# Performance work log

Hardware: AMD Instinct MI355X
Metric: run time of the kernel (lower is better)

The kernel has to match this reference:

```python
import jax, jax.numpy as jnp
import numpy as np

N = 170000      # nodes (ogbn-arxiv scale)
E = 2720000     # edges (avg degree 16)
IN, H, L, OUT = 128, 256, 4, 40
BN_EPS = 1e-5


def setup_inputs() -> dict:
    key = jax.random.key(0)
    ks = jax.random.split(key, 6)
    x = jax.random.normal(ks[0], (N, IN), jnp.float32)
    edge_index = jax.random.randint(ks[1], (2, E), 0, N, dtype=jnp.int64)
    W_in = jax.random.normal(ks[2], (IN, H), jnp.float32) * 0.05
    b_in = jnp.zeros((H,), jnp.float32)
    W_hid = jax.random.normal(ks[3], (L - 1, H, H), jnp.float32) * 0.05
    b_hid = jnp.zeros((L - 1, H), jnp.float32)
    gamma = jnp.ones((L, H), jnp.float32)
    beta = jnp.zeros((L, H), jnp.float32)
    W_out = jax.random.normal(ks[4], (L * H, OUT), jnp.float32) * 0.05
    b_out = jnp.zeros((OUT,), jnp.float32)
    return dict(x=x, edge_index=edge_index, W_in=W_in, b_in=b_in,
                W_hid=W_hid, b_hid=b_hid, gamma=gamma, beta=beta,
                W_out=W_out, b_out=b_out)


def _gcn_aggregate(h, src, dst, norm_e, inv_deg):
    # message passing with symmetric normalization + self-loop term
    msg = h[src] * norm_e[:, None]                      # [E, H] gather
    agg = jax.ops.segment_sum(msg, dst, num_segments=N)  # [N, H] scatter-add
    return agg + h * inv_deg[:, None]                   # self-loop: deg^-1


def reference(x, edge_index, W_in, b_in, W_hid, b_hid, gamma, beta, W_out, b_out):
    src, dst = edge_index[0], edge_index[1]
    # degree (incl. self-loop), PyG gcn_norm style
    deg = jax.ops.segment_sum(jnp.ones((E,), x.dtype), dst, num_segments=N) + 1.0
    dinv = jax.lax.rsqrt(deg)
    norm_e = dinv[src] * dinv[dst]
    inv_deg = 1.0 / deg

    outs = []
    h = x
    for i in range(L):
        W = W_in if i == 0 else W_hid[i - 1]
        b = b_in if i == 0 else b_hid[i - 1]
        h = _gcn_aggregate(h @ W, src, dst, norm_e, inv_deg) + b
        # BatchNorm1d (training-mode batch statistics, biased variance)
        mean = jnp.mean(h, axis=0)
        var = jnp.mean(jnp.square(h - mean), axis=0)
        h = (h - mean) * jax.lax.rsqrt(var + BN_EPS) * gamma[i] + beta[i]
        h = jax.nn.relu(h)  # dropout is identity in eval mode
        outs.append(h)

    z = jnp.concatenate(outs, axis=-1) @ W_out + b_out  # JK 'cat' -> [N, L*H] @ [L*H, OUT]
    return jax.nn.log_softmax(z, axis=-1)
```

## Files before the change

### kernel.cpp

```cpp
#include <hip/hip_runtime.h>
#include <math.h>

constexpr int kN = 170000;
constexpr int kE = 2720000;
constexpr int kFin = 128;
constexpr int kFh = 256;
constexpr int kL = 4;
constexpr int kFout = 40;

typedef __attribute__((ext_vector_type(8))) short bf16x8;
typedef __attribute__((ext_vector_type(4))) float f32x4;

__device__ __forceinline__ float jk_b2f(unsigned short u) {
    unsigned int x = ((unsigned int)u) << 16;
    float f;
    __builtin_memcpy(&f, &x, 4);
    return f;
}
__device__ __forceinline__ unsigned short jk_f2b(float f) {
    unsigned int x;
    __builtin_memcpy(&x, &f, 4);
    unsigned int r = (x + 0x7fffu + ((x >> 16) & 1u)) >> 16;
    return (unsigned short)r;
}

union U4 {
    uint4 v;
    unsigned short s[8];
};

__global__ void jk7_zero_i(int* p, int n) {
    int i = blockIdx.x * blockDim.x + threadIdx.x;
    if (i < n) p[i] = 0;
}
__global__ void jk7_zero_f(float* p, int n) {
    int i = blockIdx.x * blockDim.x + threadIdx.x;
    if (i < n) p[i] = 0.0f;
}

__global__ void jk7_detect(const int* eb, int* flag) {
    __shared__ int nz;
    if (threadIdx.x == 0) nz = 0;
    __syncthreads();
    int bad = 0;
    for (int j = 0; j < 4; j++) {
        int idx = threadIdx.x * 4 + j;
        if (eb[2 * idx + 1] != 0) bad = 1;
    }
    if (bad) atomicOr(&nz, 1);
    __syncthreads();
    if (threadIdx.x == 0) {
        flag[0] = nz ? 0 : 1;
        flag[1] = 0;
    }
}

__global__ void jk7_count(const int* eb, const int* flag, int* counts, int* rank) {
    int e = blockIdx.x * blockDim.x + threadIdx.x;
    if (e >= kE) return;
    int s64 = flag[0];
    int d = eb[(kE + e) << s64];
    rank[e] = atomicAdd(&counts[d], 1);
}

__global__ void jk7_nodeprep(const int* counts, float* dinv, float* invdeg, int* off,
                             int* cursor) {
    int n = blockIdx.x * blockDim.x + threadIdx.x;
    if (n < kN) {
        int c = counts[n];
        float deg = (float)c + 1.0f;
        dinv[n] = rsqrtf(deg);
        invdeg[n] = 1.0f / deg;
        off[n] = atomicAdd(cursor, c);
    }
}

__global__ void jk7_fill(const int* eb, const int* flag, const int* rank, const int* off,
                         const float* dinv, int2* csr) {
    int e = blockIdx.x * blockDim.x + threadIdx.x;
    if (e >= kE) return;
    int s64 = flag[0];
    int s = eb[e << s64];
    int d = eb[(kE + e) << s64];
    int p = off[d] + rank[e];
    float w = dinv[s] * dinv[d];
    csr[p] = make_int2(s, __float_as_int(w));
}

__global__ void jk7_wt(const float* W, unsigned short* Wt, int K) {
    int idx = blockIdx.x * blockDim.x + threadIdx.x;
    if (idx >= K * kFh) return;
    int c = idx / K, k = idx % K;
    Wt[idx] = jk_f2b(W[(size_t)k * kFh + c]);
}

__global__ void jk7_wtout(const float* Wout, unsigned short* Wto) {
    int idx = blockIdx.x * blockDim.x + threadIdx.x;
    if (idx >= kL * 48 * 256) return;
    int l = idx / (48 * 256);
    int rem = idx % (48 * 256);
    int col = rem >> 8, k = rem & 255;
    float wv = (col < kFout) ? Wout[(size_t)(l * kFh + k) * kFout + col] : 0.f;
    unsigned short hi = jk_f2b(wv);
    float res = wv - jk_b2f(hi);
    unsigned short lo = jk_f2b(res);
    Wto[((size_t)(l * 2 + 0) * 48 + col) * 256 + k] = hi;
    Wto[((size_t)(l * 2 + 1) * 48 + col) * 256 + k] = lo;
}

template <int MODE>
__global__ __launch_bounds__(256) void jk7_gemm(const void* Aptr, const unsigned short* Wt,
                                                unsigned short* C, int K, const float* sc,
                                                const float* sh) {
    __shared__ unsigned short As[128][40];
    __shared__ unsigned short Bs[128][40];
    __shared__ float ssc[256], ssh[256];
    int tid = threadIdx.x;
    if (MODE == 1) {
        ssc[tid] = sc[tid];
        ssh[tid] = sh[tid];
    }
    __syncthreads();
    int row0 = blockIdx.x * 128;
    int n0 = blockIdx.y * 128;
    int lane = tid & 63, w = tid >> 6;
    int wm = w >> 1, wn = w & 1;
    int lr = lane & 15, lg = lane >> 4;

    f32x4 acc[4][4];
#pragma unroll
    for (int i = 0; i < 4; i++)
#pragma unroll
        for (int j = 0; j < 4; j++) acc[i][j] = (f32x4){0.f, 0.f, 0.f, 0.f};

    int sr = tid >> 1;
    int skh = (tid & 1) * 16;

    for (int k0 = 0; k0 < K; k0 += 32) {
        {
            int row = row0 + sr;
            if (MODE == 0) {
                const float* A = (const float*)Aptr;
                unsigned short tmp[16];
                if (row < kN) {
                    const float* g = A + (size_t)row * K + k0 + skh;
#pragma unroll
                    for (int j = 0; j < 16; j++) tmp[j] = jk_f2b(g[j]);
                } else {
#pragma unroll
                    for (int j = 0; j < 16; j++) tmp[j] = 0;
                }
                *(uint4*)&As[sr][skh] = *(uint4*)&tmp[0];
                *(uint4*)&As[sr][skh + 8] = *(uint4*)&tmp[8];
            } else {
                const unsigned short* A = (const unsigned short*)Aptr;
                U4 o0, o1;
                if (row < kN) {
                    U4 u0, u1;
                    const unsigned short* g = A + (size_t)row * K + k0 + skh;
                    u0.v = *(const uint4*)g;
                    u1.v = *(const uint4*)(g + 8);
#pragma unroll
                    for (int j = 0; j < 8; j++) {
                        float v = jk_b2f(u0.s[j]) * ssc[k0 + skh + j] + ssh[k0 + skh + j];
                        o0.s[j] = jk_f2b(v > 0.f ? v : 0.f);
                    }
#pragma unroll
                    for (int j = 0; j < 8; j++) {
                        float v = jk_b2f(u1.s[j]) * ssc[k0 + skh + 8 + j] + ssh[k0 + skh + 8 + j];
                        o1.s[j] = jk_f2b(v > 0.f ? v : 0.f);
                    }
                } else {
#pragma unroll
                    for (int j = 0; j < 8; j++) { o0.s[j] = 0; o1.s[j] = 0; }
                }
                *(uint4*)&As[sr][skh] = o0.v;
                *(uint4*)&As[sr][skh + 8] = o1.v;
            }
        }
        {
            const unsigned short* g = Wt + (size_t)(n0 + sr) * K + k0 + skh;
            *(uint4*)&Bs[sr][skh] = *(const uint4*)g;
            *(uint4*)&Bs[sr][skh + 8] = *(const uint4*)(g + 8);
        }
        __syncthreads();

        bf16x8 af[4], bfr[4];
#pragma unroll
        for (int mi = 0; mi < 4; mi++)
            af[mi] = *(const bf16x8*)&As[wm * 64 + mi * 16 + lr][lg * 8];
#pragma unroll
        for (int ni = 0; ni < 4; ni++)
            bfr[ni] = *(const bf16x8*)&Bs[wn * 64 + ni * 16 + lr][lg * 8];
#pragma unroll
        for (int mi = 0; mi < 4; mi++)
#pragma unroll
            for (int ni = 0; ni < 4; ni++)
                acc[mi][ni] = __builtin_amdgcn_mfma_f32_16x16x32_bf16(af[mi], bfr[ni],
                                                                      acc[mi][ni], 0, 0, 0);
        __syncthreads();
    }

#pragma unroll
    for (int mi = 0; mi < 4; mi++) {
#pragma unroll
        for (int j = 0; j < 4; j++) {
            int row = row0 + wm * 64 + mi * 16 + lg * 4 + j;
            if (row < kN) {
#pragma unroll
                for (int ni = 0; ni < 4; ni++) {
                    int col = n0 + wn * 64 + ni * 16 + lr;
                    C[(size_t)row * kFh + col] = jk_f2b(acc[mi][ni][j]);
                }
            }
        }
    }
}

__global__ __launch_bounds__(256) void jk7_agg(const unsigned short* t, const float* bias,
                                               const int* off, const int* cnt, const int2* csr,
                                               const float* invdeg, unsigned short* h) {
    int n = blockIdx.x * 8 + (threadIdx.x >> 5);
    if (n >= kN) return;
    int c0 = (threadIdx.x & 31) * 8;

    float acc[8];
    {
        U4 u;
        u.v = *(const uint4*)(t + (size_t)n * kFh + c0);
        float sw = invdeg[n];
#pragma unroll
        for (int j = 0; j < 8; j++) acc[j] = sw * jk_b2f(u.s[j]);
    }

    int base = off[n], c = cnt[n];
    for (int i = 0; i < c; i += 4) {
        float w[4];
        U4 uu[4];
#pragma unroll
        for (int q = 0; q < 4; q++) {
            int e = i + q;
            bool v = e < c;
            int2 cw = csr[v ? base + e : base];
            w[q] = v ? __int_as_float(cw.y) : 0.0f;
            uu[q].v = *(const uint4*)(t + (size_t)cw.x * kFh + c0);
        }
#pragma unroll
        for (int q = 0; q < 4; q++)
#pragma unroll
            for (int j = 0; j < 8; j++) acc[j] += w[q] * jk_b2f(uu[q].s[j]);
    }

    U4 o;
#pragma unroll
    for (int j = 0; j < 8; j++) o.s[j] = jk_f2b(acc[j] + bias[c0 + j]);
    *(uint4*)(h + (size_t)n * kFh + c0) = o.v;
}

__global__ __launch_bounds__(256) void jk7_bnstats(const unsigned short* h, float* stats) {
    __shared__ float lsum[256], lsq[256];
    int tid = threadIdx.x;
    lsum[tid] = 0.f;
    lsq[tid] = 0.f;
    __syncthreads();
    int c0 = (tid & 31) * 8;
    int grp = tid >> 5;
    float rs[8] = {}, rq[8] = {};
    for (int n = blockIdx.x * 8 + grp; n < kN; n += gridDim.x * 8) {
        U4 u;
        u.v = *(const uint4*)(h + (size_t)n * kFh + c0);
#pragma unroll
        for (int j = 0; j < 8; j++) {
            float v = jk_b2f(u.s[j]);
            rs[j] += v;
            rq[j] += v * v;
        }
    }
#pragma unroll
    for (int j = 0; j < 8; j++) {
        atomicAdd(&lsum[c0 + j], rs[j]);
        atomicAdd(&lsq[c0 + j], rq[j]);
    }
    __syncthreads();
    atomicAdd(&stats[tid], lsum[tid]);
    atomicAdd(&stats[256 + tid], lsq[tid]);
}

__global__ void jk7_bnfinal(const float* stats, const float* gamma, const float* beta, int layer,
                            float* scale, float* shift) {
    int c = threadIdx.x;
    float mean = stats[c] / (float)kN;
    float var = stats[256 + c] / (float)kN - mean * mean;
    var = var < 0.f ? 0.f : var;
    float sc = gamma[layer * kFh + c] * rsqrtf(var + 1e-5f);
    scale[c] = sc;
    shift[c] = beta[layer * kFh + c] - mean * sc;
}

template <int FIRST, int LAST>
__global__ __launch_bounds__(256) void jk7_zacc(const unsigned short* h, const float* scale,
                                                const float* shift, const unsigned short* Wto,
                                                const float* bout, float* z, float* out) {
    __shared__ unsigned short Bs[2][48][264];
    __shared__ unsigned short As[128][40];
    __shared__ float ssc[256], ssh[256];
    int tid = threadIdx.x;
    for (int f = tid; f < 2 * 48 * 256; f += 256) {
        int hl = f / (48 * 256);
        int rem = f % (48 * 256);
        Bs[hl][rem >> 8][rem & 255] = Wto[f];
    }
    ssc[tid] = scale[tid];
    ssh[tid] = shift[tid];
    __syncthreads();

    int row0 = blockIdx.x * 128;
    int w = tid >> 6, lane = tid & 63;
    int lr = lane & 15, lg = lane >> 4;
    int sr = tid >> 1, skh = (tid & 1) * 16;

    f32x4 acc[2][3];
#pragma unroll
    for (int mi = 0; mi < 2; mi++)
#pragma unroll
        for (int ni = 0; ni < 3; ni++) acc[mi][ni] = (f32x4){0.f, 0.f, 0.f, 0.f};

    for (int k0 = 0; k0 < kFh; k0 += 32) {
        int row = row0 + sr;
        U4 o0, o1;
        if (row < kN) {
            U4 u0, u1;
            const unsigned short* g = h + (size_t)row * kFh + k0 + skh;
            u0.v = *(const uint4*)g;
            u1.v = *(const uint4*)(g + 8);
#pragma unroll
            for (int j = 0; j < 8; j++) {
                float v = jk_b2f(u0.s[j]) * ssc[k0 + skh + j] + ssh[k0 + skh + j];
                o0.s[j] = jk_f2b(v > 0.f ? v : 0.f);
            }
#pragma unroll
            for (int j = 0; j < 8; j++) {
                float v = jk_b2f(u1.s[j]) * ssc[k0 + skh + 8 + j] + ssh[k0 + skh + 8 + j];
                o1.s[j] = jk_f2b(v > 0.f ? v : 0.f);
            }
        } else {
#pragma unroll
            for (int j = 0; j < 8; j++) { o0.s[j] = 0; o1.s[j] = 0; }
        }
        *(uint4*)&As[sr][skh] = o0.v;
        *(uint4*)&As[sr][skh + 8] = o1.v;
        __syncthreads();

        bf16x8 af[2], bh[3], bl[3];
#pragma unroll
        for (int mi = 0; mi < 2; mi++)
            af[mi] = *(const bf16x8*)&As[w * 32 + mi * 16 + lr][lg * 8];
#pragma unroll
        for (int ni = 0; ni < 3; ni++) {
            bh[ni] = *(const bf16x8*)&Bs[0][ni * 16 + lr][k0 + lg * 8];
            bl[ni] = *(const bf16x8*)&Bs[1][ni * 16 + lr][k0 + lg * 8];
        }
#pragma unroll
        for (int mi = 0; mi < 2; mi++)
#pragma unroll
            for (int ni = 0; ni < 3; ni++) {
                acc[mi][ni] = __builtin_amdgcn_mfma_f32_16x16x32_bf16(af[mi], bh[ni],
                                                                      acc[mi][ni], 0, 0, 0);
                acc[mi][ni] = __builtin_amdgcn_mfma_f32_16x16x32_bf16(af[mi], bl[ni],
                                                                      acc[mi][ni], 0, 0, 0);
            }
        __syncthreads();
    }

#pragma unroll
    for (int mi = 0; mi < 2; mi++) {
#pragma unroll
        for (int j = 0; j < 4; j++) {
            int row = row0 + w * 32 + mi * 16 + lg * 4 + j;
            if (row >= kN) continue;
            if (!LAST) {
#pragma unroll
                for (int ni = 0; ni < 3; ni++) {
                    int col = ni * 16 + lr;
                    if (col < kFout) {
                        if (FIRST)
                            z[(size_t)row * kFout + col] = acc[mi][ni][j] + bout[col];
                        else
                            z[(size_t)row * kFout + col] += acc[mi][ni][j];
                    }
                }
            } else {
                const float* zp = z + (size_t)row * kFout;
                float v0 = zp[lr] + acc[mi][0][j];
                float v1 = zp[16 + lr] + acc[mi][1][j];
                float v2 = (lr < 8) ? (zp[32 + lr] + acc[mi][2][j]) : -1e30f;
                float m = fmaxf(fmaxf(v0, v1), v2);
                m = fmaxf(m, __shfl_xor(m, 1, 64));
                m = fmaxf(m, __shfl_xor(m, 2, 64));
                m = fmaxf(m, __shfl_xor(m, 4, 64));
                m = fmaxf(m, __shfl_xor(m, 8, 64));
                float s = expf(v0 - m) + expf(v1 - m) + ((lr < 8) ? expf(v2 - m) : 0.f);
                s += __shfl_xor(s, 1, 64);
                s += __shfl_xor(s, 2, 64);
                s += __shfl_xor(s, 4, 64);
                s += __shfl_xor(s, 8, 64);
                float ls = m + logf(s);
                float* op = out + (size_t)row * kFout;
                op[lr] = v0 - ls;
                op[16 + lr] = v1 - ls;
                if (lr < 8) op[32 + lr] = v2 - ls;
            }
        }
    }
}

extern "C" void kernel_launch(void* const* d_in, const int* in_sizes, int n_in,
                              void* d_out, int out_size, void* d_ws, size_t ws_size,
                              hipStream_t stream) {
    (void)in_sizes; (void)n_in; (void)out_size; (void)ws_size;
    const float* x = (const float*)d_in[0];
    const int* eb = (const int*)d_in[1];
    const float* W_in = (const float*)d_in[2];
    const float* b_in = (const float*)d_in[3];
    const float* W_hid = (const float*)d_in[4];
    const float* b_hid = (const float*)d_in[5];
    const float* gamma = (const float*)d_in[6];
    const float* beta = (const float*)d_in[7];
    const float* W_out = (const float*)d_in[8];
    const float* b_out = (const float*)d_in[9];
    float* out = (float*)d_out;

    char* p = (char*)d_ws;
    auto alloc = [&](size_t b) -> void* {
        void* r = (void*)p;
        p += (b + 255) & ~(size_t)255;
        return r;
    };
    int* flag = (int*)alloc(8);
    int* counts = (int*)alloc((size_t)kN * 4);
    int* off = (int*)alloc((size_t)kN * 4);
    float* dinv = (float*)alloc((size_t)kN * 4);
    float* invdeg = (float*)alloc((size_t)kN * 4);
    float* bnsums = (float*)alloc((size_t)kL * 512 * 4);
    float* bnss = (float*)alloc((size_t)kL * 512 * 4);
    int* rank = (int*)alloc((size_t)kE * 4);
    int2* csr = (int2*)alloc((size_t)kE * 8);
    unsigned short* hA = (unsigned short*)alloc((size_t)kN * kFh * 2);
    unsigned short* hB = (unsigned short*)alloc((size_t)kN * kFh * 2);
    float* z = (float*)alloc((size_t)kN * kFout * 4);
    unsigned short* Wt0 = (unsigned short*)alloc((size_t)kFin * kFh * 2);
    unsigned short* Wt1 = (unsigned short*)alloc((size_t)kFh * kFh * 2);
    unsigned short* Wt2 = (unsigned short*)alloc((size_t)kFh * kFh * 2);
    unsigned short* Wt3 = (unsigned short*)alloc((size_t)kFh * kFh * 2);
    unsigned short* Wto = (unsigned short*)alloc((size_t)kL * 2 * 48 * 256 * 2);

    jk7_zero_i<<<(kN + 255) / 256, 256, 0, stream>>>(counts, kN);
    jk7_zero_f<<<(kL * 512 + 255) / 256, 256, 0, stream>>>(bnsums, kL * 512);
    jk7_detect<<<1, 256, 0, stream>>>(eb, flag);
    jk7_count<<<(kE + 255) / 256, 256, 0, stream>>>(eb, flag, counts, rank);
    jk7_nodeprep<<<(kN + 255) / 256, 256, 0, stream>>>(counts, dinv, invdeg, off, flag + 1);
    jk7_fill<<<(kE + 255) / 256, 256, 0, stream>>>(eb, flag, rank, off, dinv, csr);

    jk7_wt<<<(kFin * kFh + 255) / 256, 256, 0, stream>>>(W_in, Wt0, kFin);
    jk7_wt<<<(kFh * kFh + 255) / 256, 256, 0, stream>>>(W_hid, Wt1, kFh);
    jk7_wt<<<(kFh * kFh + 255) / 256, 256, 0, stream>>>(W_hid + (size_t)kFh * kFh, Wt2, kFh);
    jk7_wt<<<(kFh * kFh + 255) / 256, 256, 0, stream>>>(W_hid + (size_t)2 * kFh * kFh, Wt3, kFh);
    jk7_wtout<<<(kL * 48 * 256 + 255) / 256, 256, 0, stream>>>(W_out, Wto);

    unsigned short* Wts[4] = {Wt0, Wt1, Wt2, Wt3};
    dim3 gg((kN + 127) / 128, 2);
    int zg = (kN + 127) / 128;
    for (int l = 0; l < kL; l++) {
        const float* b = (l == 0) ? b_in : b_hid + (size_t)(l - 1) * kFh;
        int K = (l == 0) ? kFin : kFh;
        if (l == 0) {
            jk7_gemm<0><<<gg, 256, 0, stream>>>(x, Wts[l], hA, K, nullptr, nullptr);
        } else {
            float* scp = bnss + (size_t)(l - 1) * 512;
            jk7_gemm<1><<<gg, 256, 0, stream>>>(hB, Wts[l], hA, K, scp, scp + 256);
        }
        jk7_agg<<<(kN + 7) / 8, 256, 0, stream>>>(hA, b, off, counts, csr, invdeg, hB);
        jk7_bnstats<<<1024, 256, 0, stream>>>(hB, bnsums + (size_t)l * 512);
        jk7_bnfinal<<<1, 256, 0, stream>>>(bnsums + (size_t)l * 512, gamma, beta, l,
                                           bnss + (size_t)l * 512, bnss + (size_t)l * 512 + 256);
        const unsigned short* wtl = Wto + (size_t)l * 2 * 48 * 256;
        float* sc = bnss + (size_t)l * 512;
        if (l == 0)
            jk7_zacc<1, 0><<<zg, 256, 0, stream>>>(hB, sc, sc + 256, wtl, b_out, z, out);
        else if (l < kL - 1)
            jk7_zacc<0, 0><<<zg, 256, 0, stream>>>(hB, sc, sc + 256, wtl, b_out, z, out);
        else
            jk7_zacc<0, 1><<<zg, 256, 0, stream>>>(hB, sc, sc + 256, wtl, b_out, z, out);
    }
}
```

Baseline: 1.759 ms.

## Aggregate before GEMM in first layer, vectorize CSR build, merge weight prep

Layer 0 now aggregates over the 128-wide bf16 input before multiplying by W_in, using linearity, so the gather runs over 128 channels instead of 256. The input bias is folded into the GEMM epilogue. The count and fill kernels handle four edges per thread with vector loads. The weight transposes are merged into one launch, and x is converted to bf16 once up front. Together these cut gather traffic and launch count, at the price of a changed rounding order (bf16 aggregation before the GEMM).

```diff
diff --git a/kernel.cpp b/kernel.cpp
--- a/kernel.cpp
+++ b/kernel.cpp
@@ -28,17 +28,21 @@
     uint4 v;
     unsigned short s[8];
 };
-
-__global__ void jk7_zero_i(int* p, int n) {
+union U2 {
+    uint2 v;
+    unsigned short s[4];
+};
+
+__global__ void jk8_zero_i(int* p, int n) {
     int i = blockIdx.x * blockDim.x + threadIdx.x;
     if (i < n) p[i] = 0;
 }
-__global__ void jk7_zero_f(float* p, int n) {
+__global__ void jk8_zero_f(float* p, int n) {
     int i = blockIdx.x * blockDim.x + threadIdx.x;
     if (i < n) p[i] = 0.0f;
 }
 
-__global__ void jk7_detect(const int* eb, int* flag) {
+__global__ void jk8_detect(const int* eb, int* flag) {
     __shared__ int nz;
     if (threadIdx.x == 0) nz = 0;
     __syncthreads();
@@ -55,15 +59,26 @@
     }
 }
 
-__global__ void jk7_count(const int* eb, const int* flag, int* counts, int* rank) {
-    int e = blockIdx.x * blockDim.x + threadIdx.x;
-    if (e >= kE) return;
+__global__ void jk8_count(const int* eb, const int* flag, int* counts, int* rank) {
+    int e0 = (blockIdx.x * blockDim.x + threadIdx.x) * 4;
+    if (e0 >= kE) return;
     int s64 = flag[0];
-    int d = eb[(kE + e) << s64];
-    rank[e] = atomicAdd(&counts[d], 1);
-}
-
-__global__ void jk7_nodeprep(const int* counts, float* dinv, float* invdeg, int* off,
+    int d[4];
+    if (s64) {
+        int4 c1 = *(const int4*)(eb + 2 * ((size_t)kE + e0));
+        int4 c2 = *(const int4*)(eb + 2 * ((size_t)kE + e0) + 4);
+        d[0] = c1.x; d[1] = c1.z; d[2] = c2.x; d[3] = c2.z;
+    } else {
+        int4 c1 = *(const int4*)(eb + (size_t)kE + e0);
+        d[0] = c1.x; d[1] = c1.y; d[2] = c1.z; d[3] = c1.w;
+    }
+    int r[4];
+#pragma unroll
+    for (int q = 0; q < 4; q++) r[q] = atomicAdd(&counts[d[q]], 1);
+    *(int4*)(rank + e0) = make_int4(r[0], r[1], r[2], r[3]);
+}
+
+__global__ void jk8_nodeprep(const int* counts, float* dinv, float* invdeg, int* off,
                              int* cursor) {
     int n = blockIdx.x * blockDim.x + threadIdx.x;
     if (n < kN) {
@@ -75,43 +90,73 @@
     }
 }
 
-__global__ void jk7_fill(const int* eb, const int* flag, const int* rank, const int* off,
+__global__ void jk8_fill(const int* eb, const int* flag, const int* rank, const int* off,
                          const float* dinv, int2* csr) {
-    int e = blockIdx.x * blockDim.x + threadIdx.x;
-    if (e >= kE) return;
+    int e0 = (blockIdx.x * blockDim.x + threadIdx.x) * 4;
+    if (e0 >= kE) return;
     int s64 = flag[0];
-    int s = eb[e << s64];
-    int d = eb[(kE + e) << s64];
-    int p = off[d] + rank[e];
-    float w = dinv[s] * dinv[d];
-    csr[p] = make_int2(s, __float_as_int(w));
-}
-
-__global__ void jk7_wt(const float* W, unsigned short* Wt, int K) {
+    int s[4], d[4];
+    if (s64) {
+        int4 a1 = *(const int4*)(eb + 2 * (size_t)e0);
+        int4 a2 = *(const int4*)(eb + 2 * (size_t)e0 + 4);
+        s[0] = a1.x; s[1] = a1.z; s[2] = a2.x; s[3] = a2.z;
+        int4 c1 = *(const int4*)(eb + 2 * ((size_t)kE + e0));
+        int4 c2 = *(const int4*)(eb + 2 * ((size_t)kE + e0) + 4);
+        d[0] = c1.x; d[1] = c1.z; d[2] = c2.x; d[3] = c2.z;
+    } else {
+        int4 a1 = *(const int4*)(eb + (size_t)e0);
+        s[0] = a1.x; s[1] = a1.y; s[2] = a1.z; s[3] = a1.w;
+        int4 c1 = *(const int4*)(eb + (size_t)kE + e0);
+        d[0] = c1.x; d[1] = c1.y; d[2] = c1.z; d[3] = c1.w;
+    }
+    int4 rr = *(const int4*)(rank + e0);
+    int r[4] = {rr.x, rr.y, rr.z, rr.w};
+#pragma unroll
+    for (int q = 0; q < 4; q++) {
+        int p = off[d[q]] + r[q];
+        float w = dinv[s[q]] * dinv[d[q]];
+        csr[p] = make_int2(s[q], __float_as_int(w));
+    }
+}
+
+__global__ void jk8_prepw(const float* W_in, const float* W_hid, const float* Wout,
+                          unsigned short* Wt0, unsigned short* Wt1, unsigned short* Wto) {
     int idx = blockIdx.x * blockDim.x + threadIdx.x;
-    if (idx >= K * kFh) return;
-    int c = idx / K, k = idx % K;
-    Wt[idx] = jk_f2b(W[(size_t)k * kFh + c]);
-}
-
-__global__ void jk7_wtout(const float* Wout, unsigned short* Wto) {
-    int idx = blockIdx.x * blockDim.x + threadIdx.x;
-    if (idx >= kL * 48 * 256) return;
-    int l = idx / (48 * 256);
-    int rem = idx % (48 * 256);
-    int col = rem >> 8, k = rem & 255;
-    float wv = (col < kFout) ? Wout[(size_t)(l * kFh + k) * kFout + col] : 0.f;
-    unsigned short hi = jk_f2b(wv);
-    float res = wv - jk_b2f(hi);
-    unsigned short lo = jk_f2b(res);
-    Wto[((size_t)(l * 2 + 0) * 48 + col) * 256 + k] = hi;
-    Wto[((size_t)(l * 2 + 1) * 48 + col) * 256 + k] = lo;
+    if (idx < 32768) {
+        int c = idx >> 7, k = idx & 127;
+        Wt0[idx] = jk_f2b(W_in[(size_t)k * kFh + c]);
+    } else if (idx < 32768 + 196608) {
+        int t2 = idx - 32768;
+        int l = t2 >> 16, rem = t2 & 65535;
+        int c = rem >> 8, k = rem & 255;
+        Wt1[(size_t)l * 65536 + rem] = jk_f2b(W_hid[(size_t)l * 65536 + k * kFh + c]);
+    } else if (idx < 32768 + 196608 + 49152) {
+        int t2 = idx - 32768 - 196608;
+        int l = t2 / (48 * 256), rem = t2 % (48 * 256);
+        int col = rem >> 8, k = rem & 255;
+        float wv = (col < kFout) ? Wout[(size_t)(l * kFh + k) * kFout + col] : 0.f;
+        unsigned short hi = jk_f2b(wv);
+        unsigned short lo = jk_f2b(wv - jk_b2f(hi));
+        Wto[((size_t)(l * 2 + 0) * 48 + col) * 256 + k] = hi;
+        Wto[((size_t)(l * 2 + 1) * 48 + col) * 256 + k] = lo;
+    }
+}
+
+__global__ void jk8_xb(const float* x, unsigned short* xb) {
+    int i = blockIdx.x * blockDim.x + threadIdx.x;
+    if (i >= kN * kFin / 8) return;
+    float4 a = *(const float4*)(x + (size_t)i * 8);
+    float4 b = *(const float4*)(x + (size_t)i * 8 + 4);
+    U4 o;
+    o.s[0] = jk_f2b(a.x); o.s[1] = jk_f2b(a.y); o.s[2] = jk_f2b(a.z); o.s[3] = jk_f2b(a.w);
+    o.s[4] = jk_f2b(b.x); o.s[5] = jk_f2b(b.y); o.s[6] = jk_f2b(b.z); o.s[7] = jk_f2b(b.w);
+    *(uint4*)(xb + (size_t)i * 8) = o.v;
 }
 
 template <int MODE>
-__global__ __launch_bounds__(256) void jk7_gemm(const void* Aptr, const unsigned short* Wt,
+__global__ __launch_bounds__(256) void jk8_gemm(const unsigned short* A, const unsigned short* Wt,
                                                 unsigned short* C, int K, const float* sc,
-                                                const float* sh) {
+                                                const float* sh, const float* bias) {
     __shared__ unsigned short As[128][40];
     __shared__ unsigned short Bs[128][40];
     __shared__ float ssc[256], ssh[256];
@@ -119,6 +164,8 @@
     if (MODE == 1) {
         ssc[tid] = sc[tid];
         ssh[tid] = sh[tid];
+    } else {
+        ssc[tid] = bias[tid];
     }
     __syncthreads();
     int row0 = blockIdx.x * 128;
@@ -140,20 +187,15 @@
         {
             int row = row0 + sr;
             if (MODE == 0) {
-                const float* A = (const float*)Aptr;
-                unsigned short tmp[16];
+                uint4 u0 = make_uint4(0, 0, 0, 0), u1 = make_uint4(0, 0, 0, 0);
                 if (row < kN) {
-                    const float* g = A + (size_t)row * K + k0 + skh;
-#pragma unroll
-                    for (int j = 0; j < 16; j++) tmp[j] = jk_f2b(g[j]);
-                } else {
-#pragma unroll
-                    for (int j = 0; j < 16; j++) tmp[j] = 0;
+                    const unsigned short* g = A + (size_t)row * K + k0 + skh;
+                    u0 = *(const uint4*)g;
+                    u1 = *(const uint4*)(g + 8);
                 }
-                *(uint4*)&As[sr][skh] = *(uint4*)&tmp[0];
-                *(uint4*)&As[sr][skh + 8] = *(uint4*)&tmp[8];
+                *(uint4*)&As[sr][skh] = u0;
+                *(uint4*)&As[sr][skh + 8] = u1;
             } else {
-                const unsigned short* A = (const unsigned short*)Aptr;
                 U4 o0, o1;
                 if (row < kN) {
                     U4 u0, u1;
@@ -210,54 +252,85 @@
 #pragma unroll
                 for (int ni = 0; ni < 4; ni++) {
                     int col = n0 + wn * 64 + ni * 16 + lr;
-                    C[(size_t)row * kFh + col] = jk_f2b(acc[mi][ni][j]);
+                    float v = acc[mi][ni][j];
+                    if (MODE == 0) v += ssc[col];
+                    C[(size_t)row * kFh + col] = jk_f2b(v);
                 }
             }
         }
     }
 }
 
-__global__ __launch_bounds__(256) void jk7_agg(const unsigned short* t, const float* bias,
+template <int CH, int HASB>
+__global__ __launch_bounds__(256) void jk8_agg(const unsigned short* t, const float* bias,
                                                const int* off, const int* cnt, const int2* csr,
                                                const float* invdeg, unsigned short* h) {
+    constexpr int PC = CH / 32;
+    constexpr int DEPTH = (CH == 128) ? 8 : 6;
     int n = blockIdx.x * 8 + (threadIdx.x >> 5);
     if (n >= kN) return;
-    int c0 = (threadIdx.x & 31) * 8;
-
-    float acc[8];
+    int c0 = (threadIdx.x & 31) * PC;
+
+    float acc[PC];
     {
-        U4 u;
-        u.v = *(const uint4*)(t + (size_t)n * kFh + c0);
         float sw = invdeg[n];
-#pragma unroll
-        for (int j = 0; j < 8; j++) acc[j] = sw * jk_b2f(u.s[j]);
+        if constexpr (PC == 8) {
+            U4 u;
+            u.v = *(const uint4*)(t + (size_t)n * CH + c0);
+#pragma unroll
+            for (int j = 0; j < 8; j++) acc[j] = sw * jk_b2f(u.s[j]);
+        } else {
+            U2 u;
+            u.v = *(const uint2*)(t + (size_t)n * CH + c0);
+#pragma unroll
+            for (int j = 0; j < 4; j++) acc[j] = sw * jk_b2f(u.s[j]);
+        }
     }
 
     int base = off[n], c = cnt[n];
-    for (int i = 0; i < c; i += 4) {
-        float w[4];
-        U4 uu[4];
-#pragma unroll
-        for (int q = 0; q < 4; q++) {
+    for (int i = 0; i < c; i += DEPTH) {
+        float w[DEPTH];
+        U4 u8[PC == 8 ? DEPTH : 1];
+        U2 u4[PC == 4 ? DEPTH : 1];
+#pragma unroll
+        for (int q = 0; q < DEPTH; q++) {
             int e = i + q;
             bool v = e < c;
             int2 cw = csr[v ? base + e : base];
             w[q] = v ? __int_as_float(cw.y) : 0.0f;
-            uu[q].v = *(const uint4*)(t + (size_t)cw.x * kFh + c0);
-        }
-#pragma unroll
-        for (int q = 0; q < 4; q++)
-#pragma unroll
-            for (int j = 0; j < 8; j++) acc[j] += w[q] * jk_b2f(uu[q].s[j]);
-    }
-
-    U4 o;
-#pragma unroll
-    for (int j = 0; j < 8; j++) o.s[j] = jk_f2b(acc[j] + bias[c0 + j]);
-    *(uint4*)(h + (size_t)n * kFh + c0) = o.v;
-}
-
-__global__ __launch_bounds__(256) void jk7_bnstats(const unsigned short* h, float* stats) {
+            if constexpr (PC == 8)
+                u8[q].v = *(const uint4*)(t + (size_t)cw.x * CH + c0);
+            else
+                u4[q].v = *(const uint2*)(t + (size_t)cw.x * CH + c0);
+        }
+#pragma unroll
+        for (int q = 0; q < DEPTH; q++) {
+            if constexpr (PC == 8) {
+#pragma unroll
+                for (int j = 0; j < 8; j++) acc[j] += w[q] * jk_b2f(u8[q].s[j]);
+            } else {
+#pragma unroll
+                for (int j = 0; j < 4; j++) acc[j] += w[q] * jk_b2f(u4[q].s[j]);
+            }
+        }
+    }
+
+    if constexpr (PC == 8) {
+        U4 o;
+#pragma unroll
+        for (int j = 0; j < 8; j++)
+            o.s[j] = jk_f2b(HASB ? acc[j] + bias[c0 + j] : acc[j]);
+        *(uint4*)(h + (size_t)n * CH + c0) = o.v;
+    } else {
+        U2 o;
+#pragma unroll
+        for (int j = 0; j < 4; j++)
+            o.s[j] = jk_f2b(HASB ? acc[j] + bias[c0 + j] : acc[j]);
+        *(uint2*)(h + (size_t)n * CH + c0) = o.v;
+    }
+}
+
+__global__ __launch_bounds__(256) void jk8_bnstats(const unsigned short* h, float* stats) {
     __shared__ float lsum[256], lsq[256];
     int tid = threadIdx.x;
     lsum[tid] = 0.f;
@@ -286,7 +359,7 @@
     atomicAdd(&stats[256 + tid], lsq[tid]);
 }
 
-__global__ void jk7_bnfinal(const float* stats, const float* gamma, const float* beta, int layer,
+__global__ void jk8_bnfinal(const float* stats, const float* gamma, const float* beta, int layer,
                             float* scale, float* shift) {
     int c = threadIdx.x;
     float mean = stats[c] / (float)kN;
@@ -298,7 +371,7 @@
 }
 
 template <int FIRST, int LAST>
-__global__ __launch_bounds__(256) void jk7_zacc(const unsigned short* h, const float* scale,
+__global__ __launch_bounds__(256) void jk8_zacc(const unsigned short* h, const float* scale,
                                                 const float* shift, const unsigned short* Wto,
                                                 const float* bout, float* z, float* out) {
     __shared__ unsigned short Bs[2][48][264];
@@ -449,47 +522,43 @@
     unsigned short* hB = (unsigned short*)alloc((size_t)kN * kFh * 2);
     float* z = (float*)alloc((size_t)kN * kFout * 4);
     unsigned short* Wt0 = (unsigned short*)alloc((size_t)kFin * kFh * 2);
-    unsigned short* Wt1 = (unsigned short*)alloc((size_t)kFh * kFh * 2);
-    unsigned short* Wt2 = (unsigned short*)alloc((size_t)kFh * kFh * 2);
-    unsigned short* Wt3 = (unsigned short*)alloc((size_t)kFh * kFh * 2);
+    unsigned short* Wt1 = (unsigned short*)alloc((size_t)3 * kFh * kFh * 2);
     unsigned short* Wto = (unsigned short*)alloc((size_t)kL * 2 * 48 * 256 * 2);
 
-    jk7_zero_i<<<(kN + 255) / 256, 256, 0, stream>>>(counts, kN);
-    jk7_zero_f<<<(kL * 512 + 255) / 256, 256, 0, stream>>>(bnsums, kL * 512);
-    jk7_detect<<<1, 256, 0, stream>>>(eb, flag);
-    jk7_count<<<(kE + 255) / 256, 256, 0, stream>>>(eb, flag, counts, rank);
-    jk7_nodeprep<<<(kN + 255) / 256, 256, 0, stream>>>(counts, dinv, invdeg, off, flag + 1);
-    jk7_fill<<<(kE + 255) / 256, 256, 0, stream>>>(eb, flag, rank, off, dinv, csr);
-
-    jk7_wt<<<(kFin * kFh + 255) / 256, 256, 0, stream>>>(W_in, Wt0, kFin);
-    jk7_wt<<<(kFh * kFh + 255) / 256, 256, 0, stream>>>(W_hid, Wt1, kFh);
-    jk7_wt<<<(kFh * kFh + 255) / 256, 256, 0, stream>>>(W_hid + (size_t)kFh * kFh, Wt2, kFh);
-    jk7_wt<<<(kFh * kFh + 255) / 256, 256, 0, stream>>>(W_hid + (size_t)2 * kFh * kFh, Wt3, kFh);
-    jk7_wtout<<<(kL * 48 * 256 + 255) / 256, 256, 0, stream>>>(W_out, Wto);
-
-    unsigned short* Wts[4] = {Wt0, Wt1, Wt2, Wt3};
+    jk8_zero_i<<<(kN + 255) / 256, 256, 0, stream>>>(counts, kN);
+    jk8_zero_f<<<(kL * 512 + 255) / 256, 256, 0, stream>>>(bnsums, kL * 512);
+    jk8_detect<<<1, 256, 0, stream>>>(eb, flag);
+    jk8_count<<<(kE / 4 + 255) / 256, 256, 0, stream>>>(eb, flag, counts, rank);
+    jk8_nodeprep<<<(kN + 255) / 256, 256, 0, stream>>>(counts, dinv, invdeg, off, flag + 1);
+    jk8_fill<<<(kE / 4 + 255) / 256, 256, 0, stream>>>(eb, flag, rank, off, dinv, csr);
+    jk8_prepw<<<(32768 + 196608 + 49152 + 255) / 256, 256, 0, stream>>>(W_in, W_hid, W_out,
+                                                                        Wt0, Wt1, Wto);
+    jk8_xb<<<(kN * kFin / 8 + 255) / 256, 256, 0, stream>>>(x, hB);
+    jk8_agg<128, 0><<<(kN + 7) / 8, 256, 0, stream>>>(hB, nullptr, off, counts, csr, invdeg, hA);
+
+    unsigned short* Wts[4] = {Wt0, Wt1, Wt1 + 65536, Wt1 + 131072};
     dim3 gg((kN + 127) / 128, 2);
     int zg = (kN + 127) / 128;
     for (int l = 0; l < kL; l++) {
-        const float* b = (l == 0) ? b_in : b_hid + (size_t)(l - 1) * kFh;
-        int K = (l == 0) ? kFin : kFh;
         if (l == 0) {
-            jk7_gemm<0><<<gg, 256, 0, stream>>>(x, Wts[l], hA, K, nullptr, nullptr);
+            jk8_gemm<0><<<gg, 256, 0, stream>>>(hA, Wts[0], hB, kFin, nullptr, nullptr, b_in);
         } else {
+            const float* b = b_hid + (size_t)(l - 1) * kFh;
             float* scp = bnss + (size_t)(l - 1) * 512;
-            jk7_gemm<1><<<gg, 256, 0, stream>>>(hB, Wts[l], hA, K, scp, scp + 256);
-        }
-        jk7_agg<<<(kN + 7) / 8, 256, 0, stream>>>(hA, b, off, counts, csr, invdeg, hB);
-        jk7_bnstats<<<1024, 256, 0, stream>>>(hB, bnsums + (size_t)l * 512);
-        jk7_bnfinal<<<1, 256, 0, stream>>>(bnsums + (size_t)l * 512, gamma, beta, l,
+            jk8_gemm<1><<<gg, 256, 0, stream>>>(hB, Wts[l], hA, kFh, scp, scp + 256, nullptr);
+            jk8_agg<256, 1><<<(kN + 7) / 8, 256, 0, stream>>>(hA, b, off, counts, csr, invdeg,
+                                                              hB);
+        }
+        jk8_bnstats<<<1024, 256, 0, stream>>>(hB, bnsums + (size_t)l * 512);
+        jk8_bnfinal<<<1, 256, 0, stream>>>(bnsums + (size_t)l * 512, gamma, beta, l,
                                            bnss + (size_t)l * 512, bnss + (size_t)l * 512 + 256);
         const unsigned short* wtl = Wto + (size_t)l * 2 * 48 * 256;
         float* sc = bnss + (size_t)l * 512;
         if (l == 0)
-            jk7_zacc<1, 0><<<zg, 256, 0, stream>>>(hB, sc, sc + 256, wtl, b_out, z, out);
+            jk8_zacc<1, 0><<<zg, 256, 0, stream>>>(hB, sc, sc + 256, wtl, b_out, z, out);
         else if (l < kL - 1)
-            jk7_zacc<0, 0><<<zg, 256, 0, stream>>>(hB, sc, sc + 256, wtl, b_out, z, out);
+            jk8_zacc<0, 0><<<zg, 256, 0, stream>>>(hB, sc, sc + 256, wtl, b_out, z, out);
         else
-            jk7_zacc<0, 1><<<zg, 256, 0, stream>>>(hB, sc, sc + 256, wtl, b_out, z, out);
-    }
-}
+            jk8_zacc<0, 1><<<zg, 256, 0, stream>>>(hB, sc, sc + 256, wtl, b_out, z, out);
+    }
+}
```

After: 1.656 ms. -5.9%, faster.
